# Optimization experiments

Hardware: AMD Instinct MI355X
Metric: run time of the kernel (lower is better)

Reference implementation:

```python
import jax, jax.numpy as jnp
import numpy as np

N_NODES = 50000


def setup_inputs() -> dict:
    key = jax.random.key(0)
    k1, k2, k3, k4, k5 = jax.random.split(key, 5)
    h = jax.random.normal(k1, (50000, 256), dtype=jnp.float32)
    norm = jax.random.uniform(k2, (50000, 1), dtype=jnp.float32)
    weight = jax.random.normal(k3, (256, 96), dtype=jnp.float32) * (1.0 / np.sqrt(96.0))
    src = jax.random.randint(k4, (800000,), 0, N_NODES, dtype=jnp.int64)
    dst = jax.random.randint(k5, (800000,), 0, N_NODES, dtype=jnp.int64)
    return {"h": h, "norm": norm, "weight": weight, "src": src, "dst": dst}


def reference(h, norm, weight, src, dst):
    # dense projection: [N, in] @ [in, out] -> [N, out]
    hw = jnp.matmul(h, weight)
    # pre-aggregation degree norm
    hw = hw * norm
    # copy_src + sum: gather messages from src, scatter-add into dst
    msgs = hw[src]  # [E, out]
    agg = jax.ops.segment_sum(msgs, dst, num_segments=N_NODES)
    # post-aggregation degree norm + activation
    out = jax.nn.relu(agg * norm)
    return out
```

## Files before the change

kernel.cpp:

```cpp
#include <hip/hip_runtime.h>

#define M_NODES 50000
#define KDIM    256
#define NDIM    96
#define NEDGE   800000
#define BM      64
#define GEMM_BLKS 782
#define NPB     64
#define NBUCK   782
#define CAPB    1536
#define EPB     2048
#define NBLK_SC 391
#define TOT_BLKS (GEMM_BLKS + NBLK_SC)

typedef short bf16x8 __attribute__((ext_vector_type(8)));
typedef float f32x4  __attribute__((ext_vector_type(4)));

__device__ inline unsigned short f2bf(float x) {
    unsigned u = __float_as_uint(x);
    u = (u + 0x7fffu + ((u >> 16) & 1u)) >> 16;
    return (unsigned short)u;
}
__device__ inline unsigned pack2bf(float x, float y) {
    return (unsigned)f2bf(x) | ((unsigned)f2bf(y) << 16);
}

__global__ __launch_bounds__(256) void prep_w_kernel(
    const float* __restrict__ w, unsigned short* __restrict__ wt,
    int* __restrict__ gcursor)
{
    const int b = blockIdx.x, t = threadIdx.x;
    if (b < 96) {
        wt[b * 256 + t] = f2bf(w[(size_t)t * NDIM + b]);
    } else {
        for (int i = t; i < NBUCK; i += 256) gcursor[i] = i * CAPB;
    }
}

__global__ __launch_bounds__(256) void fused_gemm_scatter_kernel(
    const float* __restrict__ h, const float* __restrict__ norm,
    const unsigned short* __restrict__ wt, unsigned short* __restrict__ hwb,
    const int* __restrict__ src, const int* __restrict__ dst,
    int* __restrict__ gcursor, unsigned* __restrict__ binned)
{
    __shared__ __align__(16) char smem[81920];

    const int tid = threadIdx.x;
    const unsigned bx = blockIdx.x;

    if (bx % 3 != 2) {
        const int gid = (int)bx - (int)((bx + 1) / 3);
        char* w_lds = smem;
        char* a_lds = smem + 49152;
        const int lane = tid & 63;
        const int wv   = tid >> 6;
        const int row0 = gid * BM;

#pragma unroll
        for (int it = 0; it < 16; ++it) {
            int idx = tid + it * 256;
            int r   = idx >> 6;
            int c4  = idx & 63;
            int row = row0 + r;
            if (row >= M_NODES) row = M_NODES - 1;
            float4 v = *reinterpret_cast<const float4*>(h + (size_t)row * KDIM + c4 * 4);
            uint2 p = make_uint2(pack2bf(v.x, v.y), pack2bf(v.z, v.w));
            *reinterpret_cast<uint2*>(a_lds + r * 512 + ((c4 * 8) ^ ((r & 7) << 4))) = p;
        }
#pragma unroll
        for (int it = 0; it < 12; ++it) {
            int idx = tid + it * 256;
            int n   = idx >> 5;
            int kb  = (idx & 31) * 16;
            uint4 v = *reinterpret_cast<const uint4*>(
                reinterpret_cast<const char*>(wt) + n * 512 + kb);
            *reinterpret_cast<uint4*>(w_lds + n * 512 + (kb ^ ((n & 7) << 4))) = v;
        }
        __syncthreads();

        f32x4 acc[6];
#pragma unroll
        for (int f = 0; f < 6; ++f) acc[f] = (f32x4){0.f, 0.f, 0.f, 0.f};

        const int ar = wv * 16 + (lane & 15);
        const int kg = lane >> 4;

#pragma unroll
        for (int s = 0; s < 8; ++s) {
            const int kb = s * 64 + kg * 16;
            bf16x8 a = *reinterpret_cast<const bf16x8*>(
                a_lds + ar * 512 + (kb ^ ((ar & 7) << 4)));
#pragma unroll
            for (int f = 0; f < 6; ++f) {
                int n = f * 16 + (lane & 15);
                bf16x8 b = *reinterpret_cast<const bf16x8*>(
                    w_lds + n * 512 + (kb ^ ((n & 7) << 4)));
                acc[f] = __builtin_amdgcn_mfma_f32_16x16x32_bf16(a, b, acc[f], 0, 0, 0);
            }
        }

        const int crow = wv * 16 + (lane >> 4) * 4;
        const int ccol = lane & 15;
#pragma unroll
        for (int r = 0; r < 4; ++r) {
            int row = row0 + crow + r;
            if (row < M_NODES) {
                float nv = norm[row];
#pragma unroll
                for (int f = 0; f < 6; ++f)
                    hwb[(size_t)row * NDIM + f * 16 + ccol] = f2bf(acc[f][r] * nv);
            }
        }
    } else {
        int* s_cnt  = reinterpret_cast<int*>(smem);
        int* s_base = s_cnt + NBUCK;
        const int blk = (int)(bx / 3);
        const int e0 = blk * EPB;
        const int e1 = (e0 + EPB < NEDGE) ? e0 + EPB : NEDGE;

        for (int i = tid; i < NBUCK; i += 256) s_cnt[i] = 0;
        __syncthreads();
        for (int e = e0 + tid; e < e1; e += 256)
            atomicAdd(&s_cnt[dst[e] >> 6], 1);
        __syncthreads();
        for (int i = tid; i < NBUCK; i += 256) {
            int c = s_cnt[i];
            s_base[i] = c ? atomicAdd(&gcursor[i], c) : 0;
        }
        __syncthreads();
        for (int i = tid; i < NBUCK; i += 256) s_cnt[i] = 0;
        __syncthreads();
        for (int e = e0 + tid; e < e1; e += 256) {
            int d = dst[e];
            int b = d >> 6;
            int pos = s_base[b] + atomicAdd(&s_cnt[b], 1);
            if (pos < (b + 1) * CAPB)
                binned[pos] = ((unsigned)(d & 63) << 16) | (unsigned)src[e];
        }
    }
}

#define ACCV(A, v)                                     \
    A[0] += __uint_as_float((v).x << 16);              \
    A[1] += __uint_as_float((v).x & 0xffff0000u);      \
    A[2] += __uint_as_float((v).y << 16);              \
    A[3] += __uint_as_float((v).y & 0xffff0000u);      \
    A[4] += __uint_as_float((v).z << 16);              \
    A[5] += __uint_as_float((v).z & 0xffff0000u);      \
    A[6] += __uint_as_float((v).w << 16);              \
    A[7] += __uint_as_float((v).w & 0xffff0000u);

__global__ __launch_bounds__(256) void csr_agg_kernel(
    const unsigned* __restrict__ binned, const int* __restrict__ gcursor,
    const unsigned short* __restrict__ hwb, const float* __restrict__ norm,
    float* __restrict__ out)
{
    __shared__ unsigned eL[CAPB];
    __shared__ unsigned short oL[CAPB];
    __shared__ int cnt[NPB];
    __shared__ int pfxE[NPB];

    const int b  = blockIdx.x;
    const int t  = threadIdx.x;
    const int e0 = b * CAPB;
    int cntE = gcursor[b] - e0;
    if (cntE > CAPB) cntE = CAPB;

    for (int i = t; i < cntE; i += 256) eL[i] = binned[e0 + i];
    if (t < NPB) cnt[t] = 0;
    __syncthreads();
    for (int i = t; i < cntE; i += 256)
        atomicAdd(&cnt[(eL[i] >> 16) & 63], 1);
    __syncthreads();
    if (t < NPB) {
        int v = cnt[t];
        int x = v;
#pragma unroll
        for (int st = 1; st < 64; st <<= 1) {
            int o = __shfl_up(x, st, 64);
            if (t >= st) x += o;
        }
        int ex = x - v;
        pfxE[t] = ex;
        cnt[t]  = ex;
    }
    __syncthreads();
    for (int i = t; i < cntE; i += 256) {
        unsigned v = eL[i];
        int d = (v >> 16) & 63;
        int p = atomicAdd(&cnt[d], 1);
        oL[p] = (unsigned short)(v & 0xffffu);
    }
    __syncthreads();

#pragma unroll
    for (int pass = 0; pass < 3; ++pass) {
        const int u     = pass * 256 + t;
        const int node  = u / 12;
        const int c8    = u - node * 12;
        const int gnode = b * NPB + node;
        if (gnode < M_NODES) {
            const int s0 = pfxE[node];
            const int s1 = cnt[node];
            float acc[8]  = {0.f, 0.f, 0.f, 0.f, 0.f, 0.f, 0.f, 0.f};
            float acc2[8] = {0.f, 0.f, 0.f, 0.f, 0.f, 0.f, 0.f, 0.f};
            int e = s0;
            for (; e + 4 <= s1; e += 4) {
                int a0 = oL[e], a1 = oL[e + 1], a2 = oL[e + 2], a3 = oL[e + 3];
                uint4 v0 = *reinterpret_cast<const uint4*>(hwb + (size_t)a0 * NDIM + c8 * 8);
                uint4 v1 = *reinterpret_cast<const uint4*>(hwb + (size_t)a1 * NDIM + c8 * 8);
                uint4 v2 = *reinterpret_cast<const uint4*>(hwb + (size_t)a2 * NDIM + c8 * 8);
                uint4 v3 = *reinterpret_cast<const uint4*>(hwb + (size_t)a3 * NDIM + c8 * 8);
                ACCV(acc, v0); ACCV(acc2, v1); ACCV(acc, v2); ACCV(acc2, v3);
            }
            for (; e < s1; ++e) {
                int a0 = oL[e];
                uint4 v0 = *reinterpret_cast<const uint4*>(hwb + (size_t)a0 * NDIM + c8 * 8);
                ACCV(acc, v0);
            }
            const float nv = norm[gnode];
            float4 o0, o1;
            o0.x = fmaxf((acc[0] + acc2[0]) * nv, 0.f);
            o0.y = fmaxf((acc[1] + acc2[1]) * nv, 0.f);
            o0.z = fmaxf((acc[2] + acc2[2]) * nv, 0.f);
            o0.w = fmaxf((acc[3] + acc2[3]) * nv, 0.f);
            o1.x = fmaxf((acc[4] + acc2[4]) * nv, 0.f);
            o1.y = fmaxf((acc[5] + acc2[5]) * nv, 0.f);
            o1.z = fmaxf((acc[6] + acc2[6]) * nv, 0.f);
            o1.w = fmaxf((acc[7] + acc2[7]) * nv, 0.f);
            float4* po = reinterpret_cast<float4*>(out + (size_t)gnode * NDIM + c8 * 8);
            po[0] = o0; po[1] = o1;
        }
    }
}

extern "C" void kernel_launch(void* const* d_in, const int* in_sizes, int n_in,
                              void* d_out, int out_size, void* d_ws, size_t ws_size,
                              hipStream_t stream)
{
    const float* h    = (const float*)d_in[0];
    const float* norm = (const float*)d_in[1];
    const float* w    = (const float*)d_in[2];
    const int*   src  = (const int*)d_in[3];
    const int*   dst  = (const int*)d_in[4];
    float* out = (float*)d_out;

    unsigned short* hwb = (unsigned short*)d_ws;
    unsigned short* wt  = hwb + (size_t)M_NODES * NDIM;
    int* gcursor = (int*)(wt + KDIM * NDIM);
    unsigned* binned = (unsigned*)(gcursor + 800);

    prep_w_kernel<<<97, 256, 0, stream>>>(w, wt, gcursor);
    fused_gemm_scatter_kernel<<<TOT_BLKS, 256, 0, stream>>>(
        h, norm, wt, hwb, src, dst, gcursor, binned);
    csr_agg_kernel<<<NBUCK, 256, 0, stream>>>(binned, gcursor, hwb, norm, out);
}
```

Before: 63.92 us.

## Load GEMM tiles via global_load_lds, halve row tile, schedule scatter blocks first

The GEMM portion now uses direct global-to-LDS loads for both the fp32 activation tile and the pre-swizzled bf16 weight, bypassing registers. The fp32-to-bf16 conversion moves to after the LDS read. The GEMM row tile shrinks from 64 to 32 rows, with waves split across output column groups. Binning blocks are placed ahead of GEMM blocks instead of interleaved. The weight is pre-swizzled at prep time to match the LDS layout. The intent is to cut register staging and raise parallelism, at the cost of twice the LDS footprint for A and more blocks that each reload the weight.

```diff
diff --git a/kernel.cpp b/kernel.cpp
--- a/kernel.cpp
+++ b/kernel.cpp
@@ -4,14 +4,14 @@
 #define KDIM    256
 #define NDIM    96
 #define NEDGE   800000
-#define BM      64
-#define GEMM_BLKS 782
+#define BMG     32
+#define GEMM_BLKS 1563
 #define NPB     64
 #define NBUCK   782
 #define CAPB    1536
 #define EPB     2048
 #define NBLK_SC 391
-#define TOT_BLKS (GEMM_BLKS + NBLK_SC)
+#define TOT_BLKS (NBLK_SC + GEMM_BLKS)
 
 typedef short bf16x8 __attribute__((ext_vector_type(8)));
 typedef float f32x4  __attribute__((ext_vector_type(4)));
@@ -25,13 +25,19 @@
     return (unsigned)f2bf(x) | ((unsigned)f2bf(y) << 16);
 }
 
+__device__ inline void gload_lds16(const void* g, void* l) {
+    __builtin_amdgcn_global_load_lds(
+        (const __attribute__((address_space(1))) void*)g,
+        (__attribute__((address_space(3))) void*)l, 16, 0, 0);
+}
+
 __global__ __launch_bounds__(256) void prep_w_kernel(
     const float* __restrict__ w, unsigned short* __restrict__ wt,
     int* __restrict__ gcursor)
 {
     const int b = blockIdx.x, t = threadIdx.x;
     if (b < 96) {
-        wt[b * 256 + t] = f2bf(w[(size_t)t * NDIM + b]);
+        wt[b * 256 + (t ^ ((b & 7) << 3))] = f2bf(w[(size_t)t * NDIM + b]);
     } else {
         for (int i = t; i < NBUCK; i += 256) gcursor[i] = i * CAPB;
     }
@@ -48,58 +54,62 @@
     const int tid = threadIdx.x;
     const unsigned bx = blockIdx.x;
 
-    if (bx % 3 != 2) {
-        const int gid = (int)bx - (int)((bx + 1) / 3);
-        char* w_lds = smem;
-        char* a_lds = smem + 49152;
+    if (bx >= NBLK_SC) {
+        const int gid = (int)bx - NBLK_SC;
+        char* a_lds = smem;
+        char* w_lds = smem + 32768;
         const int lane = tid & 63;
         const int wv   = tid >> 6;
-        const int row0 = gid * BM;
-
-#pragma unroll
-        for (int it = 0; it < 16; ++it) {
-            int idx = tid + it * 256;
-            int r   = idx >> 6;
-            int c4  = idx & 63;
-            int row = row0 + r;
-            if (row >= M_NODES) row = M_NODES - 1;
-            float4 v = *reinterpret_cast<const float4*>(h + (size_t)row * KDIM + c4 * 4);
-            uint2 p = make_uint2(pack2bf(v.x, v.y), pack2bf(v.z, v.w));
-            *reinterpret_cast<uint2*>(a_lds + r * 512 + ((c4 * 8) ^ ((r & 7) << 4))) = p;
+        const int row0 = gid * BMG;
+
+#pragma unroll
+        for (int it = 0; it < 8; ++it) {
+            const int r = wv * 8 + it;
+            int gr = row0 + r;
+            if (gr >= M_NODES) gr = M_NODES - 1;
+            const char* srcp = reinterpret_cast<const char*>(h + (size_t)gr * KDIM)
+                             + ((lane ^ (r & 7)) << 4);
+            gload_lds16(srcp, a_lds + r * 1024);
         }
 #pragma unroll
         for (int it = 0; it < 12; ++it) {
-            int idx = tid + it * 256;
-            int n   = idx >> 5;
-            int kb  = (idx & 31) * 16;
-            uint4 v = *reinterpret_cast<const uint4*>(
-                reinterpret_cast<const char*>(wt) + n * 512 + kb);
-            *reinterpret_cast<uint4*>(w_lds + n * 512 + (kb ^ ((n & 7) << 4))) = v;
-        }
-        __syncthreads();
-
-        f32x4 acc[6];
-#pragma unroll
-        for (int f = 0; f < 6; ++f) acc[f] = (f32x4){0.f, 0.f, 0.f, 0.f};
-
-        const int ar = wv * 16 + (lane & 15);
+            const int off = wv * 12288 + it * 1024;
+            gload_lds16(reinterpret_cast<const char*>(wt) + off + lane * 16,
+                        w_lds + off);
+        }
+        __syncthreads();
+
+        f32x4 acc[3];
+#pragma unroll
+        for (int f = 0; f < 3; ++f) acc[f] = (f32x4){0.f, 0.f, 0.f, 0.f};
+
+        const int ar = (wv & 1) * 16 + (lane & 15);
         const int kg = lane >> 4;
+        const int f0 = (wv >> 1) * 3;
+        const int a7 = ar & 7;
 
 #pragma unroll
         for (int s = 0; s < 8; ++s) {
+            const int c0 = s * 8 + kg * 2;
+            float4 p = *reinterpret_cast<const float4*>(
+                a_lds + ar * 1024 + ((c0 ^ a7) << 4));
+            float4 q = *reinterpret_cast<const float4*>(
+                a_lds + ar * 1024 + (((c0 + 1) ^ a7) << 4));
+            union { bf16x8 v; unsigned u[4]; } a;
+            a.u[0] = pack2bf(p.x, p.y); a.u[1] = pack2bf(p.z, p.w);
+            a.u[2] = pack2bf(q.x, q.y); a.u[3] = pack2bf(q.z, q.w);
+
             const int kb = s * 64 + kg * 16;
-            bf16x8 a = *reinterpret_cast<const bf16x8*>(
-                a_lds + ar * 512 + (kb ^ ((ar & 7) << 4)));
-#pragma unroll
-            for (int f = 0; f < 6; ++f) {
-                int n = f * 16 + (lane & 15);
+#pragma unroll
+            for (int ff = 0; ff < 3; ++ff) {
+                const int n = (f0 + ff) * 16 + (lane & 15);
                 bf16x8 b = *reinterpret_cast<const bf16x8*>(
                     w_lds + n * 512 + (kb ^ ((n & 7) << 4)));
-                acc[f] = __builtin_amdgcn_mfma_f32_16x16x32_bf16(a, b, acc[f], 0, 0, 0);
-            }
-        }
-
-        const int crow = wv * 16 + (lane >> 4) * 4;
+                acc[ff] = __builtin_amdgcn_mfma_f32_16x16x32_bf16(a.v, b, acc[ff], 0, 0, 0);
+            }
+        }
+
+        const int crow = (wv & 1) * 16 + (lane >> 4) * 4;
         const int ccol = lane & 15;
 #pragma unroll
         for (int r = 0; r < 4; ++r) {
@@ -107,14 +117,14 @@
             if (row < M_NODES) {
                 float nv = norm[row];
 #pragma unroll
-                for (int f = 0; f < 6; ++f)
-                    hwb[(size_t)row * NDIM + f * 16 + ccol] = f2bf(acc[f][r] * nv);
+                for (int ff = 0; ff < 3; ++ff)
+                    hwb[(size_t)row * NDIM + (f0 + ff) * 16 + ccol] = f2bf(acc[ff][r] * nv);
             }
         }
     } else {
         int* s_cnt  = reinterpret_cast<int*>(smem);
         int* s_base = s_cnt + NBUCK;
-        const int blk = (int)(bx / 3);
+        const int blk = (int)bx;
         const int e0 = blk * EPB;
         const int e1 = (e0 + EPB < NEDGE) ? e0 + EPB : NEDGE;
 
```

Measured after the change: 69.34 us. 8.5% more time.
